# Optimization experiments

Hardware: AMD Instinct MI355X
Metric: run time of the kernel (lower is better)

Reference implementation:

```python
import jax, jax.numpy as jnp
import numpy as np

DIM = 192
HEADS = 6
HEAD_DIM = DIM // HEADS
WS = 8            # window size
N = WS * WS       # tokens per window
IN_CC = 16        # top-k kept keys per query
B, H, W = 8, 64, 64
NEG = -100.0      # value used by the torch code for masked logits
EPS_NORM = 1e-12  # F.normalize eps
EPS_LN = 1e-5     # nn.LayerNorm eps


def _rel_pos_index(ws):
    coords = np.stack(np.meshgrid(np.arange(ws), np.arange(ws), indexing='ij'))  # (2,ws,ws)
    cf = coords.reshape(2, -1)
    rel = (cf[:, :, None] - cf[:, None, :]).transpose(1, 2, 0).astype(np.int64)  # (N,N,2)
    rel[:, :, 0] += ws - 1
    rel[:, :, 1] += ws - 1
    rel[:, :, 0] *= 2 * ws - 1
    return jnp.asarray(rel.sum(-1))  # (N,N) indices into (2ws-1)^2 table

REL_IDX = _rel_pos_index(WS)


def _layer_norm(x, g, b):
    mu = jnp.mean(x, -1, keepdims=True)
    var = jnp.mean(jnp.square(x - mu), -1, keepdims=True)
    return (x - mu) * jax.lax.rsqrt(var + EPS_LN) * g + b


def _l2n(x):
    n = jnp.sqrt(jnp.sum(jnp.square(x), -1, keepdims=True))
    return x / jnp.maximum(n, EPS_NORM)


def setup_inputs() -> dict:
    key = jax.random.key(0)
    ks = jax.random.split(key, 8)
    s = 0.02
    return {
        'x': jax.random.normal(ks[0], (B, DIM, H, W), jnp.float32),
        'norm1_g': jnp.ones((DIM,), jnp.float32),
        'norm1_b': jnp.zeros((DIM,), jnp.float32),
        'qkv_w': jax.random.normal(ks[1], (3 * DIM, DIM), jnp.float32) * s,
        'qkv_b': jnp.zeros((3 * DIM,), jnp.float32),
        'proj_w': jax.random.normal(ks[2], (DIM, DIM), jnp.float32) * s,
        'proj_b': jnp.zeros((DIM,), jnp.float32),
        'rpb_table': jax.random.normal(ks[3], ((2 * WS - 1) ** 2, HEADS), jnp.float32) * s,
        'temperature': jnp.ones((HEADS, 1, 1), jnp.float32),
        'norm2_g': jnp.ones((DIM,), jnp.float32),
        'norm2_b': jnp.zeros((DIM,), jnp.float32),
        'fc1_w': jax.random.normal(ks[4], (4 * DIM, DIM), jnp.float32) * s,
        'fc1_b': jnp.zeros((4 * DIM,), jnp.float32),
        'fc2_w': jax.random.normal(ks[5], (DIM, 4 * DIM), jnp.float32) * s,
        'fc2_b': jnp.zeros((DIM,), jnp.float32),
    }


def reference(x, norm1_g, norm1_b, qkv_w, qkv_b, proj_w, proj_b, rpb_table,
              temperature, norm2_g, norm2_b, fc1_w, fc1_b, fc2_w, fc2_b):
    b, c, h, w = x.shape
    # (B,C,H,W) -> (B,L,C), pre-norm (note: the torch code norms the shortcut too)
    xs = jnp.transpose(x.reshape(b, c, h * w), (0, 2, 1))
    shortcut = _layer_norm(xs, norm1_g, norm1_b)  # (B,L,C)

    # window partition: (B,H,W,C) -> (B*nWh*nWw, N, C); shift_size=0, no padding (H,W % WS == 0)
    xin = shortcut.reshape(b, h // WS, WS, w // WS, WS, c)
    xin = jnp.transpose(xin, (0, 1, 3, 2, 4, 5)).reshape(-1, N, c)
    B_ = xin.shape[0]

    qkv = (xin @ qkv_w.T + qkv_b).reshape(B_, N, 3, HEADS, HEAD_DIM)
    qkv = jnp.transpose(qkv, (2, 0, 3, 1, 4))  # (3, B_, h, N, d)
    q, k, v = qkv[0], qkv[1], qkv[2]

    # cosine attention with learned per-head temperature
    attn = jnp.einsum('bhnd,bhmd->bhnm', _l2n(q), _l2n(k)) * temperature  # (B_,h,N,N)

    # top-k sparsification: keep IN_CC largest logits per query (threshold == kth value;
    # equivalent to the torch topk+scatter mask for distinct values)
    kth = jax.lax.top_k(attn, IN_CC)[0][..., -1:]
    attn = jnp.where(attn >= kth, attn, NEG)

    # relative position bias gather: (N,N,h) -> (h,N,N)
    rpb = jnp.transpose(rpb_table[REL_IDX], (2, 0, 1))
    attn = jax.nn.softmax(attn + rpb[None], axis=-1)

    out = jnp.einsum('bhnm,bhmd->bhnd', attn, v)
    out = jnp.transpose(out, (0, 2, 1, 3)).reshape(B_, N, c)
    out = out @ proj_w.T + proj_b

    # window reverse -> (B, L, C)
    out = out.reshape(b, h // WS, w // WS, WS, WS, c)
    out = jnp.transpose(out, (0, 1, 3, 2, 4, 5)).reshape(b, h * w, c)

    x2 = shortcut + out  # drop_path = identity (eval)
    hdn = _layer_norm(x2, norm2_g, norm2_b)
    hdn = jax.nn.gelu(hdn @ fc1_w.T + fc1_b, approximate=False) @ fc2_w.T + fc2_b
    x2 = x2 + hdn

    # back to (B,C,H,W)
    return jnp.transpose(x2, (0, 2, 1)).reshape(b, c, h, w)
```

## Files before the change

kernel.cpp:

```cpp
#include <hip/hip_runtime.h>
#include <hip/hip_bf16.h>
#include <math.h>

#define DIM     192
#define HEADS   6
#define HEAD_DIM 32
#define NTOK    64
#define IN_CC   16
#define TTOT    32768
#define NWIN    512

using bf16x8 = __attribute__((ext_vector_type(8))) short;
using f32x4  = __attribute__((ext_vector_type(4))) float;
typedef unsigned short ushort_t;

__device__ __forceinline__ ushort_t f2b(float f) {
    unsigned u = __float_as_uint(f);
    u += 0x7fffu + ((u >> 16) & 1u);
    return (ushort_t)(u >> 16);
}
__device__ __forceinline__ unsigned pk2(float a, float b) {
    return (unsigned)f2b(a) | ((unsigned)f2b(b) << 16);
}

__global__ __launch_bounds__(256) void cvt_all_kernel(
    const float* __restrict__ s0, const float* __restrict__ s1,
    const float* __restrict__ s2, const float* __restrict__ s3,
    ushort_t* __restrict__ d0, ushort_t* __restrict__ d1,
    ushort_t* __restrict__ d2, ushort_t* __restrict__ d3)
{
    const int bid = blockIdx.x;
    const float* src; ushort_t* dst; int off, K;
    if (bid < 108)      { src = s0; dst = d0; off = bid;       K = 192; }
    else if (bid < 144) { src = s1; dst = d1; off = bid - 108; K = 192; }
    else if (bid < 288) { src = s2; dst = d2; off = bid - 144; K = 192; }
    else                { src = s3; dst = d3; off = bid - 288; K = 768; }
    const int K8 = K >> 3;
    const int d  = (off * 256 + threadIdx.x) * 4;
    const int frag = d >> 7, win = d & 127;
    const int m16w = win >> 3, k7 = win & 7;
    const int oblk = frag / K8, kblk = frag - oblk * K8;
    const int o = oblk * 16 + m16w, k = kblk * 8 + k7;
    float4 v = *(const float4*)(src + (size_t)o * K + k);
    ushort4 ov;
    ov.x = f2b(v.x); ov.y = f2b(v.y); ov.z = f2b(v.z); ov.w = f2b(v.w);
    *(ushort4*)(dst + d) = ov;
}

__global__ __launch_bounds__(256) void ln1_kernel(
    const float* __restrict__ x, const float* __restrict__ g,
    const float* __restrict__ bb, float* __restrict__ outp,
    ushort_t* __restrict__ outh)
{
    __shared__ float xs[64][193];
    __shared__ float mu_s[64], rs_s[64];
    __shared__ float gs[192], bs[192];
    const int tid = threadIdx.x;
    const int t0  = blockIdx.x * 64;
    const int b   = t0 >> 12;
    const int hw0 = t0 & 4095;
    if (tid < 192) { gs[tid] = g[tid]; bs[tid] = bb[tid]; }
    const int tok = tid & 63, qq = tid >> 6;
    const float* xb = x + (size_t)b * (DIM * 4096) + hw0 + tok;
    #pragma unroll
    for (int it = 0; it < 48; ++it) {
        int c = it * 4 + qq;
        xs[tok][c] = xb[(size_t)c * 4096];
    }
    __syncthreads();
    const int tok2 = tid >> 2, p = tid & 3;
    float sum = 0.f;
    #pragma unroll
    for (int c = 0; c < 48; ++c) sum += xs[tok2][p * 48 + c];
    sum += __shfl_xor(sum, 1);
    sum += __shfl_xor(sum, 2);
    const float m = sum * (1.0f / 192.0f);
    float ss = 0.f;
    #pragma unroll
    for (int c = 0; c < 48; ++c) { float d = xs[tok2][p * 48 + c] - m; ss += d * d; }
    ss += __shfl_xor(ss, 1);
    ss += __shfl_xor(ss, 2);
    if (p == 0) {
        mu_s[tok2] = m;
        rs_s[tok2] = 1.0f / sqrtf(ss * (1.0f / 192.0f) + 1e-5f);
    }
    __syncthreads();
    float* ob = outp + (size_t)t0 * DIM;
    ushort_t* obh = outh + (size_t)t0 * DIM;
    #pragma unroll
    for (int it = 0; it < 48; ++it) {
        int idx = it * 256 + tid;
        int tk = idx / 192, c = idx % 192;
        float v = (xs[tk][c] - mu_s[tk]) * rs_s[tk] * gs[c] + bs[c];
        ob[idx] = v;
        obh[idx] = f2b(v);
    }
}

__global__ __launch_bounds__(256) void gemm_mfma(
    const ushort_t* __restrict__ A, const ushort_t* __restrict__ Wf,
    const float* __restrict__ bias, const float* __restrict__ res,
    float* __restrict__ outf, ushort_t* __restrict__ outh,
    int N, int K, int epi)
{
    __shared__ __align__(16) float Ct[4][32][68];
    const int tid  = threadIdx.x;
    const int wave = tid >> 6, lane = tid & 63;
    const int m16 = lane & 15, quad = lane >> 4;
    const int t0 = (blockIdx.x * 4 + wave) * 64, o0 = blockIdx.y * 64;
    const int K8 = K >> 3;
    float (*Cw)[68] = Ct[wave];

    f32x4 acc[4][4];
    #pragma unroll
    for (int i = 0; i < 4; ++i)
        #pragma unroll
        for (int j = 0; j < 4; ++j)
            acc[i][j] = (f32x4)(0.0f);

    const ushort_t* Ab = A + (size_t)t0 * K + quad * 8;
    const ushort_t* Wb = Wf + (size_t)(o0 >> 4) * K8 * 128 + m16 * 8;
    for (int ks = 0; ks < K; ks += 32) {
        bf16x8 af[4], wv[4];
        #pragma unroll
        for (int i = 0; i < 4; ++i)
            af[i] = *(const bf16x8*)(Ab + (size_t)(16 * i + m16) * K + ks);
        #pragma unroll
        for (int j = 0; j < 4; ++j)
            wv[j] = *(const bf16x8*)(Wb + (size_t)(j * K8 + (ks >> 3) + quad) * 128);
        #pragma unroll
        for (int i = 0; i < 4; ++i)
            #pragma unroll
            for (int j = 0; j < 4; ++j)
                acc[i][j] = __builtin_amdgcn_mfma_f32_16x16x32_bf16(wv[j], af[i], acc[i][j], 0, 0, 0);
    }

    float4 bj[4];
    #pragma unroll
    for (int j = 0; j < 4; ++j)
        bj[j] = *(const float4*)&bias[o0 + 16 * j + quad * 4];

    #pragma unroll
    for (int p = 0; p < 2; ++p) {
        #pragma unroll
        for (int ih = 0; ih < 2; ++ih) {
            const int i = 2 * p + ih;
            #pragma unroll
            for (int j = 0; j < 4; ++j) {
                f32x4 v = acc[i][j];
                v[0] += bj[j].x; v[1] += bj[j].y; v[2] += bj[j].z; v[3] += bj[j].w;
                *(f32x4*)&Cw[ih * 16 + m16][16 * j + quad * 4] = v;
            }
        }
        if (epi == 3) {
            #pragma unroll
            for (int q = 0; q < 4; ++q) {
                const int idx = q * 64 + lane;
                const int row = idx >> 3, c8 = (idx & 7) * 8;
                float4 f0 = *(const float4*)&Cw[row][c8];
                float4 f1 = *(const float4*)&Cw[row][c8 + 4];
                uint4 w;
                w.x = pk2(f0.x, f0.y); w.y = pk2(f0.z, f0.w);
                w.z = pk2(f1.x, f1.y); w.w = pk2(f1.z, f1.w);
                *(uint4*)&outh[(size_t)(t0 + p * 32 + row) * N + o0 + c8] = w;
            }
        } else {
            #pragma unroll
            for (int q = 0; q < 8; ++q) {
                const int idx = q * 64 + lane;
                const int row = idx >> 4, c4 = (idx & 15) * 4;
                float4 vv = *(const float4*)&Cw[row][c4];
                const size_t gidx = (size_t)(t0 + p * 32 + row) * N + o0 + c4;
                if (epi == 1) {
                    const float4 rv = *(const float4*)&res[gidx];
                    vv.x += rv.x; vv.y += rv.y; vv.z += rv.z; vv.w += rv.w;
                }
                *(float4*)&outf[gidx] = vv;
            }
        }
    }
}

__global__ __launch_bounds__(384) void attn_proj_fused(
    const ushort_t* __restrict__ qkvh, const float* __restrict__ rpb_table,
    const float* __restrict__ temp, const ushort_t* __restrict__ wpf,
    const float* __restrict__ proj_b, const float* __restrict__ shortcut,
    float* __restrict__ x2)
{
    __shared__ __align__(16) char smem[96768];
    const int tid  = threadIdx.x;
    const int wave = tid >> 6, n = tid & 63;
    char* arena = smem + wave * 16128;
    ushort_t* Qh  = (ushort_t*)arena;
    ushort_t* Kh  = (ushort_t*)(arena + 5120);
    float*    Ss  = (float*)arena;
    ushort_t* Pl  = (ushort_t*)arena;
    ushort_t* Vt  = (ushort_t*)(arena + 10240);
    float*    ksb = (float*)(arena + 14848);
    float*    rpb = (float*)(arena + 15104);
    ushort_t (*AoT)[200] = (ushort_t(*)[200])smem;
    float* Cww = (float*)(smem + 25600 + wave * 9216);

    const int win = blockIdx.x;
    const int h   = wave;
    const int b   = win >> 6;
    const int wh  = (win >> 3) & 7, ww = win & 7;
    const int i1  = n >> 3, j1 = n & 7;
    const int t   = b * 4096 + (wh * 8 + i1) * 64 + (ww * 8 + j1);
    const ushort_t* base = qkvh + (size_t)t * 576 + h * 32;
    const int m16 = n & 15, quad = n >> 4;

    unsigned qu[16], ku[16], vu[16];
    #pragma unroll
    for (int c = 0; c < 4; ++c) {
        ((uint4*)qu)[c] = *(const uint4*)(base + 8 * c);
        ((uint4*)ku)[c] = *(const uint4*)(base + 192 + 8 * c);
        ((uint4*)vu)[c] = *(const uint4*)(base + 384 + 8 * c);
    }
    float sq = 0.f, sk = 0.f;
    #pragma unroll
    for (int c = 0; c < 16; ++c) {
        float a0 = __uint_as_float(qu[c] << 16);
        float a1 = __uint_as_float(qu[c] & 0xffff0000u);
        sq += a0 * a0 + a1 * a1;
        float b0 = __uint_as_float(ku[c] << 16);
        float b1 = __uint_as_float(ku[c] & 0xffff0000u);
        sk += b0 * b0 + b1 * b1;
    }
    const float qs  = temp[h] / fmaxf(sqrtf(sq), 1e-12f);
    const float ksc = 1.0f / fmaxf(sqrtf(sk), 1e-12f);

    #pragma unroll
    for (int c = 0; c < 4; ++c) {
        *(uint4*)&Qh[n * 40 + 8 * c] = ((uint4*)qu)[c];
        *(uint4*)&Kh[n * 40 + 8 * c] = ((uint4*)ku)[c];
    }
    const int vslot = 4 * m16 + quad;
    #pragma unroll
    for (int d = 0; d < 16; ++d) {
        Vt[(2 * d) * 72 + vslot]     = (ushort_t)(vu[d] & 0xffffu);
        Vt[(2 * d + 1) * 72 + vslot] = (ushort_t)(vu[d] >> 16);
    }
    ksb[vslot] = ksc;
    for (int r = n; r < 225; r += 64) rpb[r] = rpb_table[r * 6 + h];
    __syncthreads();

    bf16x8 aq[4], bk[4];
    #pragma unroll
    for (int i = 0; i < 4; ++i) aq[i] = *(const bf16x8*)&Qh[(16*i + m16) * 40 + quad * 8];
    #pragma unroll
    for (int j = 0; j < 4; ++j) bk[j] = *(const bf16x8*)&Kh[(16*j + m16) * 40 + quad * 8];
    f32x4 acc[4][4];
    #pragma unroll
    for (int i = 0; i < 4; ++i)
        #pragma unroll
        for (int j = 0; j < 4; ++j)
            acc[i][j] = __builtin_amdgcn_mfma_f32_16x16x32_bf16(aq[i], bk[j], (f32x4)(0.0f), 0, 0, 0);
    __syncthreads();

    float s[64];
    #pragma unroll
    for (int i = 0; i < 2; ++i)
        #pragma unroll
        for (int r = 0; r < 4; ++r) {
            f32x4 vv = { acc[i][0][r], acc[i][1][r], acc[i][2][r], acc[i][3][r] };
            *(f32x4*)&Ss[(16 * i + 4 * quad + r) * 68 + 4 * m16] = vv;
        }
    __syncthreads();
    if (n < 32) {
        #pragma unroll
        for (int c = 0; c < 16; ++c)
            *(float4*)&s[4 * c] = *(const float4*)&Ss[n * 68 + 4 * c];
    }
    __syncthreads();
    #pragma unroll
    for (int i = 2; i < 4; ++i)
        #pragma unroll
        for (int r = 0; r < 4; ++r) {
            f32x4 vv = { acc[i][0][r], acc[i][1][r], acc[i][2][r], acc[i][3][r] };
            *(f32x4*)&Ss[(16 * (i - 2) + 4 * quad + r) * 68 + 4 * m16] = vv;
        }
    __syncthreads();
    if (n >= 32) {
        #pragma unroll
        for (int c = 0; c < 16; ++c)
            *(float4*)&s[4 * c] = *(const float4*)&Ss[(n - 32) * 68 + 4 * c];
    }

    #pragma unroll
    for (int c = 0; c < 16; ++c) {
        float4 kv = *(const float4*)&ksb[4 * c];
        s[4*c+0] *= qs * kv.x; s[4*c+1] *= qs * kv.y;
        s[4*c+2] *= qs * kv.z; s[4*c+3] *= qs * kv.w;
    }

    float thr = 1e30f;
    for (int it = 0; it < IN_CC; ++it) {
        float mx = -1e30f;
        #pragma unroll
        for (int m = 0; m < 64; ++m) {
            float vv = (s[m] < thr) ? s[m] : -1e30f;
            mx = fmaxf(mx, vv);
        }
        thr = mx;
    }

    const int basen = i1 * 15 + j1;
    float mx = -1e30f;
    #pragma unroll
    for (int c = 0; c < 64; ++c) {
        const int m = 16 * (c & 3) + (c >> 2);
        const int i2 = m >> 3, j2 = m & 7;
        float vv = ((s[c] >= thr) ? s[c] : -100.0f)
                 + rpb[basen + (7 - i2) * 15 + (7 - j2)];
        s[c] = vv;
        mx = fmaxf(mx, vv);
    }
    float sum = 0.f;
    #pragma unroll
    for (int c = 0; c < 64; ++c) { float e = __expf(s[c] - mx); s[c] = e; sum += e; }
    const float inv = 1.0f / sum;
    #pragma unroll
    for (int c = 0; c < 64; ++c) s[c] *= inv;

    __syncthreads();
    #pragma unroll
    for (int gix = 0; gix < 8; ++gix) {
        uint4 w;
        w.x = pk2(s[8*gix+0], s[8*gix+1]); w.y = pk2(s[8*gix+2], s[8*gix+3]);
        w.z = pk2(s[8*gix+4], s[8*gix+5]); w.w = pk2(s[8*gix+6], s[8*gix+7]);
        *(uint4*)&Pl[n * 72 + 8 * gix] = w;
    }
    __syncthreads();

    f32x4 o[4][2];
    #pragma unroll
    for (int i = 0; i < 4; ++i)
        #pragma unroll
        for (int j2 = 0; j2 < 2; ++j2)
            o[i][j2] = (f32x4)(0.0f);
    #pragma unroll
    for (int kh = 0; kh < 64; kh += 32) {
        bf16x8 pa[4], vb[2];
        #pragma unroll
        for (int i = 0; i < 4; ++i)
            pa[i] = *(const bf16x8*)&Pl[(16*i + m16) * 72 + kh + quad * 8];
        #pragma unroll
        for (int j2 = 0; j2 < 2; ++j2)
            vb[j2] = *(const bf16x8*)&Vt[(16*j2 + m16) * 72 + kh + quad * 8];
        #pragma unroll
        for (int i = 0; i < 4; ++i)
            #pragma unroll
            for (int j2 = 0; j2 < 2; ++j2)
                o[i][j2] = __builtin_amdgcn_mfma_f32_16x16x32_bf16(pa[i], vb[j2], o[i][j2], 0, 0, 0);
    }
    __syncthreads();

    #pragma unroll
    for (int i = 0; i < 4; ++i) {
        #pragma unroll
        for (int r = 0; r < 4; ++r) {
            const int row = 16 * i + 4 * quad + r;
            AoT[row][h * 32 + m16]      = f2b(o[i][0][r]);
            AoT[row][h * 32 + 16 + m16] = f2b(o[i][1][r]);
        }
    }
    __syncthreads();

    f32x4 pacc[4][2];
    #pragma unroll
    for (int i = 0; i < 4; ++i)
        #pragma unroll
        for (int j = 0; j < 2; ++j)
            pacc[i][j] = (f32x4)(0.0f);
    const ushort_t* Wb = wpf + (size_t)(wave * 2) * 24 * 128 + m16 * 8;
    for (int ks = 0; ks < 192; ks += 32) {
        bf16x8 af[4], wv[2];
        #pragma unroll
        for (int i = 0; i < 4; ++i)
            af[i] = *(const bf16x8*)&AoT[16 * i + m16][quad * 8 + ks];
        #pragma unroll
        for (int j = 0; j < 2; ++j)
            wv[j] = *(const bf16x8*)(Wb + (size_t)(j * 24 + (ks >> 3) + quad) * 128);
        #pragma unroll
        for (int i = 0; i < 4; ++i)
            #pragma unroll
            for (int j = 0; j < 2; ++j)
                pacc[i][j] = __builtin_amdgcn_mfma_f32_16x16x32_bf16(wv[j], af[i], pacc[i][j], 0, 0, 0);
    }

    float4 bj[2];
    #pragma unroll
    for (int j = 0; j < 2; ++j)
        bj[j] = *(const float4*)&proj_b[wave * 32 + 16 * j + quad * 4];
    #pragma unroll
    for (int i = 0; i < 4; ++i)
        #pragma unroll
        for (int j = 0; j < 2; ++j) {
            f32x4 v = pacc[i][j];
            v[0] += bj[j].x; v[1] += bj[j].y; v[2] += bj[j].z; v[3] += bj[j].w;
            *(f32x4*)&Cww[(16 * i + m16) * 36 + 16 * j + quad * 4] = v;
        }

    #pragma unroll
    for (int q = 0; q < 8; ++q) {
        const int idx = q * 64 + n;
        const int row = idx >> 3, c4 = (idx & 7) * 4;
        const int ii = row >> 3, jj = row & 7;
        const int tt = b * 4096 + (wh * 8 + ii) * 64 + ww * 8 + jj;
        float4 vv = *(const float4*)&Cww[row * 36 + c4];
        const float4 rv = *(const float4*)&shortcut[(size_t)tt * DIM + wave * 32 + c4];
        vv.x += rv.x; vv.y += rv.y; vv.z += rv.z; vv.w += rv.w;
        *(float4*)&x2[(size_t)tt * DIM + wave * 32 + c4] = vv;
    }
}

__global__ __launch_bounds__(256) void mlp_fused(
    const float* __restrict__ x2, const ushort_t* __restrict__ w1f,
    const ushort_t* __restrict__ w2f, const float* __restrict__ fc1_b,
    const float* __restrict__ fc2_b, const float* __restrict__ g2,
    const float* __restrict__ b2, float* __restrict__ outp)
{
    __shared__ __align__(16) char smem[43008];
    ushort_t (*h_h)[200] = (ushort_t(*)[200])smem;
    ushort_t (*a1c)[136] = (ushort_t(*)[136])(smem + 25600);
    float* gs  = (float*)(smem + 25600);
    float* bs  = gs + 192;

    const int tid  = threadIdx.x;
    const int wave = tid >> 6, lane = tid & 63;
    const int m16 = lane & 15, quad = lane >> 4;
    const int t0 = blockIdx.x * 64;
    const int b   = t0 >> 12;
    const int hw0 = t0 & 4095;

    if (tid < 192) { gs[tid] = g2[tid]; bs[tid] = b2[tid]; }
    __syncthreads();
    {
        const int tok = tid >> 2, p = tid & 3;
        const float* rp = x2 + (size_t)(t0 + tok) * DIM + p * 48;
        float xv[48];
        #pragma unroll
        for (int c4 = 0; c4 < 12; ++c4)
            *(float4*)&xv[c4 * 4] = *(const float4*)(rp + c4 * 4);
        float sum = 0.f;
        #pragma unroll
        for (int c = 0; c < 48; ++c) sum += xv[c];
        sum += __shfl_xor(sum, 1);
        sum += __shfl_xor(sum, 2);
        const float m = sum * (1.0f / 192.0f);
        float ss = 0.f;
        #pragma unroll
        for (int c = 0; c < 48; ++c) { float d = xv[c] - m; ss += d * d; }
        ss += __shfl_xor(ss, 1);
        ss += __shfl_xor(ss, 2);
        const float rs = 1.0f / sqrtf(ss * (1.0f / 192.0f) + 1e-5f);
        ushort_t* hp = &h_h[tok][p * 48];
        #pragma unroll
        for (int c2 = 0; c2 < 24; ++c2) {
            float v0 = (xv[2*c2]   - m) * rs * gs[p * 48 + 2*c2]   + bs[p * 48 + 2*c2];
            float v1 = (xv[2*c2+1] - m) * rs * gs[p * 48 + 2*c2+1] + bs[p * 48 + 2*c2+1];
            *(unsigned*)(hp + 2 * c2) = pk2(v0, v1);
        }
    }
    __syncthreads();

    f32x4 acc2[4][3];
    #pragma unroll
    for (int i = 0; i < 4; ++i)
        #pragma unroll
        for (int j = 0; j < 3; ++j)
            acc2[i][j] = (f32x4)(0.0f);

    for (int c = 0; c < 6; ++c) {
        f32x4 acc1[4][2];
        #pragma unroll
        for (int i = 0; i < 4; ++i)
            #pragma unroll
            for (int j = 0; j < 2; ++j)
                acc1[i][j] = (f32x4)(0.0f);
        const ushort_t* Wb1 = w1f + (size_t)(c * 8 + wave * 2) * 24 * 128 + m16 * 8;
        for (int ks = 0; ks < 192; ks += 32) {
            bf16x8 af[4], wv[2];
            #pragma unroll
            for (int i = 0; i < 4; ++i)
                af[i] = *(const bf16x8*)&h_h[16 * i + m16][quad * 8 + ks];
            #pragma unroll
            for (int j = 0; j < 2; ++j)
                wv[j] = *(const bf16x8*)(Wb1 + (size_t)(j * 24 + (ks >> 3) + quad) * 128);
            #pragma unroll
            for (int i = 0; i < 4; ++i)
                #pragma unroll
                for (int j = 0; j < 2; ++j)
                    acc1[i][j] = __builtin_amdgcn_mfma_f32_16x16x32_bf16(wv[j], af[i], acc1[i][j], 0, 0, 0);
        }
        #pragma unroll
        for (int j = 0; j < 2; ++j) {
            const int o = c * 128 + wave * 32 + 16 * j + quad * 4;
            const float4 bv = *(const float4*)&fc1_b[o];
            #pragma unroll
            for (int i = 0; i < 4; ++i) {
                f32x4 v = acc1[i][j];
                v[0] += bv.x; v[1] += bv.y; v[2] += bv.z; v[3] += bv.w;
                #pragma unroll
                for (int r = 0; r < 4; ++r) {
                    float xg = v[r];
                    float e1 = __expf(xg * (1.5957691f + 0.0713548f * xg * xg)) + 1.0f;
                    v[r] = xg - xg * __builtin_amdgcn_rcpf(e1);
                }
                uint2 pkd;
                pkd.x = pk2(v[0], v[1]); pkd.y = pk2(v[2], v[3]);
                *(uint2*)&a1c[16 * i + m16][wave * 32 + 16 * j + quad * 4] = pkd;
            }
        }
        __syncthreads();
        const ushort_t* Wb2 = w2f + (size_t)(wave * 3) * 96 * 128 + m16 * 8;
        for (int ks = 0; ks < 128; ks += 32) {
            bf16x8 af2[4], wv2[3];
            #pragma unroll
            for (int i = 0; i < 4; ++i)
                af2[i] = *(const bf16x8*)&a1c[16 * i + m16][quad * 8 + ks];
            #pragma unroll
            for (int j = 0; j < 3; ++j)
                wv2[j] = *(const bf16x8*)(Wb2 + (size_t)(j * 96 + c * 16 + (ks >> 3) + quad) * 128);
            #pragma unroll
            for (int i = 0; i < 4; ++i)
                #pragma unroll
                for (int j = 0; j < 3; ++j)
                    acc2[i][j] = __builtin_amdgcn_mfma_f32_16x16x32_bf16(wv2[j], af2[i], acc2[i][j], 0, 0, 0);
        }
        __syncthreads();
    }

    float (*Cw)[68] = (float(*)[68])(smem + wave * 8704);
    float4 b2j[3];
    #pragma unroll
    for (int j = 0; j < 3; ++j)
        b2j[j] = *(const float4*)&fc2_b[wave * 48 + 16 * j + quad * 4];
    #pragma unroll
    for (int p = 0; p < 2; ++p) {
        #pragma unroll
        for (int ih = 0; ih < 2; ++ih) {
            const int i = 2 * p + ih;
            #pragma unroll
            for (int j = 0; j < 3; ++j) {
                f32x4 v = acc2[i][j];
                v[0] += b2j[j].x; v[1] += b2j[j].y; v[2] += b2j[j].z; v[3] += b2j[j].w;
                *(f32x4*)&Cw[ih * 16 + m16][16 * j + quad * 4] = v;
            }
        }
        #pragma unroll
        for (int q = 0; q < 6; ++q) {
            const int idx = q * 64 + lane;
            const int cc = idx >> 3, t4 = (idx & 7) * 4;
            const int o  = wave * 48 + cc;
            const int tb = t0 + p * 32 + t4;
            float4 vv;
            vv.x = Cw[t4 + 0][cc] + x2[(size_t)(tb + 0) * DIM + o];
            vv.y = Cw[t4 + 1][cc] + x2[(size_t)(tb + 1) * DIM + o];
            vv.z = Cw[t4 + 2][cc] + x2[(size_t)(tb + 2) * DIM + o];
            vv.w = Cw[t4 + 3][cc] + x2[(size_t)(tb + 3) * DIM + o];
            *(float4*)&outp[(size_t)b * (DIM * 4096) + (size_t)o * 4096
                            + hw0 + p * 32 + t4] = vv;
        }
    }
}

extern "C" void kernel_launch(void* const* d_in, const int* in_sizes, int n_in,
                              void* d_out, int out_size, void* d_ws, size_t ws_size,
                              hipStream_t stream)
{
    const float* x        = (const float*)d_in[0];
    const float* norm1_g  = (const float*)d_in[1];
    const float* norm1_b  = (const float*)d_in[2];
    const float* qkv_w    = (const float*)d_in[3];
    const float* qkv_b    = (const float*)d_in[4];
    const float* proj_w   = (const float*)d_in[5];
    const float* proj_b   = (const float*)d_in[6];
    const float* rpbt     = (const float*)d_in[7];
    const float* temp     = (const float*)d_in[8];
    const float* norm2_g  = (const float*)d_in[9];
    const float* norm2_b  = (const float*)d_in[10];
    const float* fc1_w    = (const float*)d_in[11];
    const float* fc1_b    = (const float*)d_in[12];
    const float* fc2_w    = (const float*)d_in[13];
    const float* fc2_b    = (const float*)d_in[14];
    float* out = (float*)d_out;

    char* wsb = (char*)d_ws;
    float*    shortcut   = (float*)wsb;
    ushort_t* shortcut_h = (ushort_t*)(wsb + 25165824);
    ushort_t* qkvh       = (ushort_t*)(wsb + 37748736);
    float*    x2         = (float*)(wsb + 88080384);
    ushort_t* wq  = (ushort_t*)(wsb + 125829120);
    ushort_t* wp  = wq + 110592;
    ushort_t* w1  = wp + 36864;
    ushort_t* w2  = w1 + 147456;

    hipLaunchKernelGGL(cvt_all_kernel, dim3(432), dim3(256), 0, stream,
                       qkv_w, proj_w, fc1_w, fc2_w, wq, wp, w1, w2);

    hipLaunchKernelGGL(ln1_kernel, dim3(TTOT / 64), dim3(256), 0, stream,
                       x, norm1_g, norm1_b, shortcut, shortcut_h);
    hipLaunchKernelGGL(gemm_mfma, dim3(TTOT / 256, 9), dim3(256), 0, stream,
                       shortcut_h, wq, qkv_b, (const float*)nullptr,
                       (float*)nullptr, qkvh, 576, 192, 3);
    hipLaunchKernelGGL(attn_proj_fused, dim3(NWIN), dim3(384), 0, stream,
                       qkvh, rpbt, temp, wp, proj_b, shortcut, x2);
    hipLaunchKernelGGL(mlp_fused, dim3(TTOT / 64), dim3(256), 0, stream,
                       x2, w1, w2, fc1_b, fc2_b, norm2_g, norm2_b, out);
}
```

Before: 217.3 us.

## Fuse QKV projection into windowed attention kernel and drop fp32 shortcut

Moves the QKV GEMM inside the per-window attention kernel, where each wave computes its head's Q, K and V directly into shared memory. This removes the separate GEMM launch and the large bf16 qkv intermediate. The LayerNorm kernel no longer writes an fp32 shortcut; the residual is read from the bf16 normalized tensor, trading precision for bandwidth. Several block barriers are removed, relying on per-wave private shared arenas.

```diff
diff --git a/kernel.cpp b/kernel.cpp
--- a/kernel.cpp
+++ b/kernel.cpp
@@ -21,6 +21,9 @@
 }
 __device__ __forceinline__ unsigned pk2(float a, float b) {
     return (unsigned)f2b(a) | ((unsigned)f2b(b) << 16);
+}
+__device__ __forceinline__ float b2f(ushort_t u) {
+    return __uint_as_float(((unsigned)u) << 16);
 }
 
 __global__ __launch_bounds__(256) void cvt_all_kernel(
@@ -49,8 +52,7 @@
 
 __global__ __launch_bounds__(256) void ln1_kernel(
     const float* __restrict__ x, const float* __restrict__ g,
-    const float* __restrict__ bb, float* __restrict__ outp,
-    ushort_t* __restrict__ outh)
+    const float* __restrict__ bb, ushort_t* __restrict__ outh)
 {
     __shared__ float xs[64][193];
     __shared__ float mu_s[64], rs_s[64];
@@ -85,119 +87,33 @@
         rs_s[tok2] = 1.0f / sqrtf(ss * (1.0f / 192.0f) + 1e-5f);
     }
     __syncthreads();
-    float* ob = outp + (size_t)t0 * DIM;
     ushort_t* obh = outh + (size_t)t0 * DIM;
     #pragma unroll
     for (int it = 0; it < 48; ++it) {
         int idx = it * 256 + tid;
         int tk = idx / 192, c = idx % 192;
-        float v = (xs[tk][c] - mu_s[tk]) * rs_s[tk] * gs[c] + bs[c];
-        ob[idx] = v;
-        obh[idx] = f2b(v);
-    }
-}
-
-__global__ __launch_bounds__(256) void gemm_mfma(
-    const ushort_t* __restrict__ A, const ushort_t* __restrict__ Wf,
-    const float* __restrict__ bias, const float* __restrict__ res,
-    float* __restrict__ outf, ushort_t* __restrict__ outh,
-    int N, int K, int epi)
+        obh[idx] = f2b((xs[tk][c] - mu_s[tk]) * rs_s[tk] * gs[c] + bs[c]);
+    }
+}
+
+__global__ __launch_bounds__(384) void attn_fused(
+    const ushort_t* __restrict__ sc_h, const ushort_t* __restrict__ wqf,
+    const float* __restrict__ qkv_b, const float* __restrict__ rpb_table,
+    const float* __restrict__ temp, const ushort_t* __restrict__ wpf,
+    const float* __restrict__ proj_b, float* __restrict__ x2)
 {
-    __shared__ __align__(16) float Ct[4][32][68];
-    const int tid  = threadIdx.x;
-    const int wave = tid >> 6, lane = tid & 63;
-    const int m16 = lane & 15, quad = lane >> 4;
-    const int t0 = (blockIdx.x * 4 + wave) * 64, o0 = blockIdx.y * 64;
-    const int K8 = K >> 3;
-    float (*Cw)[68] = Ct[wave];
-
-    f32x4 acc[4][4];
-    #pragma unroll
-    for (int i = 0; i < 4; ++i)
-        #pragma unroll
-        for (int j = 0; j < 4; ++j)
-            acc[i][j] = (f32x4)(0.0f);
-
-    const ushort_t* Ab = A + (size_t)t0 * K + quad * 8;
-    const ushort_t* Wb = Wf + (size_t)(o0 >> 4) * K8 * 128 + m16 * 8;
-    for (int ks = 0; ks < K; ks += 32) {
-        bf16x8 af[4], wv[4];
-        #pragma unroll
-        for (int i = 0; i < 4; ++i)
-            af[i] = *(const bf16x8*)(Ab + (size_t)(16 * i + m16) * K + ks);
-        #pragma unroll
-        for (int j = 0; j < 4; ++j)
-            wv[j] = *(const bf16x8*)(Wb + (size_t)(j * K8 + (ks >> 3) + quad) * 128);
-        #pragma unroll
-        for (int i = 0; i < 4; ++i)
-            #pragma unroll
-            for (int j = 0; j < 4; ++j)
-                acc[i][j] = __builtin_amdgcn_mfma_f32_16x16x32_bf16(wv[j], af[i], acc[i][j], 0, 0, 0);
-    }
-
-    float4 bj[4];
-    #pragma unroll
-    for (int j = 0; j < 4; ++j)
-        bj[j] = *(const float4*)&bias[o0 + 16 * j + quad * 4];
-
-    #pragma unroll
-    for (int p = 0; p < 2; ++p) {
-        #pragma unroll
-        for (int ih = 0; ih < 2; ++ih) {
-            const int i = 2 * p + ih;
-            #pragma unroll
-            for (int j = 0; j < 4; ++j) {
-                f32x4 v = acc[i][j];
-                v[0] += bj[j].x; v[1] += bj[j].y; v[2] += bj[j].z; v[3] += bj[j].w;
-                *(f32x4*)&Cw[ih * 16 + m16][16 * j + quad * 4] = v;
-            }
-        }
-        if (epi == 3) {
-            #pragma unroll
-            for (int q = 0; q < 4; ++q) {
-                const int idx = q * 64 + lane;
-                const int row = idx >> 3, c8 = (idx & 7) * 8;
-                float4 f0 = *(const float4*)&Cw[row][c8];
-                float4 f1 = *(const float4*)&Cw[row][c8 + 4];
-                uint4 w;
-                w.x = pk2(f0.x, f0.y); w.y = pk2(f0.z, f0.w);
-                w.z = pk2(f1.x, f1.y); w.w = pk2(f1.z, f1.w);
-                *(uint4*)&outh[(size_t)(t0 + p * 32 + row) * N + o0 + c8] = w;
-            }
-        } else {
-            #pragma unroll
-            for (int q = 0; q < 8; ++q) {
-                const int idx = q * 64 + lane;
-                const int row = idx >> 4, c4 = (idx & 15) * 4;
-                float4 vv = *(const float4*)&Cw[row][c4];
-                const size_t gidx = (size_t)(t0 + p * 32 + row) * N + o0 + c4;
-                if (epi == 1) {
-                    const float4 rv = *(const float4*)&res[gidx];
-                    vv.x += rv.x; vv.y += rv.y; vv.z += rv.z; vv.w += rv.w;
-                }
-                *(float4*)&outf[gidx] = vv;
-            }
-        }
-    }
-}
-
-__global__ __launch_bounds__(384) void attn_proj_fused(
-    const ushort_t* __restrict__ qkvh, const float* __restrict__ rpb_table,
-    const float* __restrict__ temp, const ushort_t* __restrict__ wpf,
-    const float* __restrict__ proj_b, const float* __restrict__ shortcut,
-    float* __restrict__ x2)
-{
-    __shared__ __align__(16) char smem[96768];
+    __shared__ __align__(16) char smem[98304];
     const int tid  = threadIdx.x;
     const int wave = tid >> 6, n = tid & 63;
-    char* arena = smem + wave * 16128;
+    char* arena = smem + wave * 16384;
     ushort_t* Qh  = (ushort_t*)arena;
     ushort_t* Kh  = (ushort_t*)(arena + 5120);
     float*    Ss  = (float*)arena;
     ushort_t* Pl  = (ushort_t*)arena;
     ushort_t* Vt  = (ushort_t*)(arena + 10240);
     float*    ksb = (float*)(arena + 14848);
-    float*    rpb = (float*)(arena + 15104);
+    float*    qnb = (float*)(arena + 15104);
+    float*    rpb = (float*)(arena + 15360);
     ushort_t (*AoT)[200] = (ushort_t(*)[200])smem;
     float* Cww = (float*)(smem + 25600 + wave * 9216);
 
@@ -206,44 +122,82 @@
     const int b   = win >> 6;
     const int wh  = (win >> 3) & 7, ww = win & 7;
     const int i1  = n >> 3, j1 = n & 7;
-    const int t   = b * 4096 + (wh * 8 + i1) * 64 + (ww * 8 + j1);
-    const ushort_t* base = qkvh + (size_t)t * 576 + h * 32;
     const int m16 = n & 15, quad = n >> 4;
 
-    unsigned qu[16], ku[16], vu[16];
-    #pragma unroll
-    for (int c = 0; c < 4; ++c) {
-        ((uint4*)qu)[c] = *(const uint4*)(base + 8 * c);
-        ((uint4*)ku)[c] = *(const uint4*)(base + 192 + 8 * c);
-        ((uint4*)vu)[c] = *(const uint4*)(base + 384 + 8 * c);
-    }
-    float sq = 0.f, sk = 0.f;
-    #pragma unroll
-    for (int c = 0; c < 16; ++c) {
-        float a0 = __uint_as_float(qu[c] << 16);
-        float a1 = __uint_as_float(qu[c] & 0xffff0000u);
-        sq += a0 * a0 + a1 * a1;
-        float b0 = __uint_as_float(ku[c] << 16);
-        float b1 = __uint_as_float(ku[c] & 0xffff0000u);
-        sk += b0 * b0 + b1 * b1;
-    }
-    const float qs  = temp[h] / fmaxf(sqrtf(sq), 1e-12f);
-    const float ksc = 1.0f / fmaxf(sqrtf(sk), 1e-12f);
-
-    #pragma unroll
-    for (int c = 0; c < 4; ++c) {
-        *(uint4*)&Qh[n * 40 + 8 * c] = ((uint4*)qu)[c];
-        *(uint4*)&Kh[n * 40 + 8 * c] = ((uint4*)ku)[c];
-    }
-    const int vslot = 4 * m16 + quad;
-    #pragma unroll
-    for (int d = 0; d < 16; ++d) {
-        Vt[(2 * d) * 72 + vslot]     = (ushort_t)(vu[d] & 0xffffu);
-        Vt[(2 * d + 1) * 72 + vslot] = (ushort_t)(vu[d] >> 16);
-    }
-    ksb[vslot] = ksc;
     for (int r = n; r < 225; r += 64) rpb[r] = rpb_table[r * 6 + h];
-    __syncthreads();
+
+    int trow[4];
+    #pragma unroll
+    for (int i = 0; i < 4; ++i) {
+        const int row = 16 * i + m16;
+        trow[i] = b * 4096 + (wh * 8 + (row >> 3)) * 64 + ww * 8 + (row & 7);
+    }
+
+    #pragma unroll
+    for (int part = 0; part < 3; ++part) {
+        const int o0 = part * 192 + h * 32;
+        f32x4 pa[4][2];
+        #pragma unroll
+        for (int i = 0; i < 4; ++i)
+            #pragma unroll
+            for (int j = 0; j < 2; ++j)
+                pa[i][j] = (f32x4)(0.0f);
+        const ushort_t* Wb = wqf + (size_t)(o0 >> 4) * 24 * 128 + m16 * 8;
+        for (int ks = 0; ks < 192; ks += 32) {
+            bf16x8 af[4], wv[2];
+            #pragma unroll
+            for (int i = 0; i < 4; ++i)
+                af[i] = *(const bf16x8*)(sc_h + (size_t)trow[i] * 192 + ks + quad * 8);
+            #pragma unroll
+            for (int j = 0; j < 2; ++j)
+                wv[j] = *(const bf16x8*)(Wb + (size_t)(j * 24 + (ks >> 3) + quad) * 128);
+            #pragma unroll
+            for (int i = 0; i < 4; ++i)
+                #pragma unroll
+                for (int j = 0; j < 2; ++j)
+                    pa[i][j] = __builtin_amdgcn_mfma_f32_16x16x32_bf16(wv[j], af[i], pa[i][j], 0, 0, 0);
+        }
+        float4 bv0 = *(const float4*)&qkv_b[o0 + quad * 4];
+        float4 bv1 = *(const float4*)&qkv_b[o0 + 16 + quad * 4];
+        float ssq[4] = {0.f, 0.f, 0.f, 0.f};
+        #pragma unroll
+        for (int i = 0; i < 4; ++i) {
+            f32x4 v0 = pa[i][0], v1 = pa[i][1];
+            v0[0] += bv0.x; v0[1] += bv0.y; v0[2] += bv0.z; v0[3] += bv0.w;
+            v1[0] += bv1.x; v1[1] += bv1.y; v1[2] += bv1.z; v1[3] += bv1.w;
+            if (part < 2) {
+                #pragma unroll
+                for (int r = 0; r < 4; ++r)
+                    ssq[i] += v0[r] * v0[r] + v1[r] * v1[r];
+                ushort_t* dst = (part == 0) ? Qh : Kh;
+                uint2 w0, w1;
+                w0.x = pk2(v0[0], v0[1]); w0.y = pk2(v0[2], v0[3]);
+                w1.x = pk2(v1[0], v1[1]); w1.y = pk2(v1[2], v1[3]);
+                *(uint2*)&dst[(16 * i + m16) * 40 + quad * 4]      = w0;
+                *(uint2*)&dst[(16 * i + m16) * 40 + 16 + quad * 4] = w1;
+            } else {
+                #pragma unroll
+                for (int r = 0; r < 4; ++r) {
+                    Vt[(quad * 4 + r) * 72 + 4 * m16 + i]      = f2b(v0[r]);
+                    Vt[(16 + quad * 4 + r) * 72 + 4 * m16 + i] = f2b(v1[r]);
+                }
+            }
+        }
+        if (part < 2) {
+            #pragma unroll
+            for (int i = 0; i < 4; ++i) {
+                ssq[i] += __shfl_xor(ssq[i], 16);
+                ssq[i] += __shfl_xor(ssq[i], 32);
+            }
+            if (quad == 0) {
+                #pragma unroll
+                for (int i = 0; i < 4; ++i) {
+                    if (part == 0) qnb[16 * i + m16] = ssq[i];
+                    else           ksb[4 * m16 + i]  = 1.0f / fmaxf(sqrtf(ssq[i]), 1e-12f);
+                }
+            }
+        }
+    }
 
     bf16x8 aq[4], bk[4];
     #pragma unroll
@@ -256,7 +210,6 @@
         #pragma unroll
         for (int j = 0; j < 4; ++j)
             acc[i][j] = __builtin_amdgcn_mfma_f32_16x16x32_bf16(aq[i], bk[j], (f32x4)(0.0f), 0, 0, 0);
-    __syncthreads();
 
     float s[64];
     #pragma unroll
@@ -266,13 +219,11 @@
             f32x4 vv = { acc[i][0][r], acc[i][1][r], acc[i][2][r], acc[i][3][r] };
             *(f32x4*)&Ss[(16 * i + 4 * quad + r) * 68 + 4 * m16] = vv;
         }
-    __syncthreads();
     if (n < 32) {
         #pragma unroll
         for (int c = 0; c < 16; ++c)
             *(float4*)&s[4 * c] = *(const float4*)&Ss[n * 68 + 4 * c];
     }
-    __syncthreads();
     #pragma unroll
     for (int i = 2; i < 4; ++i)
         #pragma unroll
@@ -280,13 +231,13 @@
             f32x4 vv = { acc[i][0][r], acc[i][1][r], acc[i][2][r], acc[i][3][r] };
             *(f32x4*)&Ss[(16 * (i - 2) + 4 * quad + r) * 68 + 4 * m16] = vv;
         }
-    __syncthreads();
     if (n >= 32) {
         #pragma unroll
         for (int c = 0; c < 16; ++c)
             *(float4*)&s[4 * c] = *(const float4*)&Ss[(n - 32) * 68 + 4 * c];
     }
 
+    const float qs = temp[h] / fmaxf(sqrtf(qnb[n]), 1e-12f);
     #pragma unroll
     for (int c = 0; c < 16; ++c) {
         float4 kv = *(const float4*)&ksb[4 * c];
@@ -323,7 +274,6 @@
     #pragma unroll
     for (int c = 0; c < 64; ++c) s[c] *= inv;
 
-    __syncthreads();
     #pragma unroll
     for (int gix = 0; gix < 8; ++gix) {
         uint4 w;
@@ -331,7 +281,6 @@
         w.z = pk2(s[8*gix+4], s[8*gix+5]); w.w = pk2(s[8*gix+6], s[8*gix+7]);
         *(uint4*)&Pl[n * 72 + 8 * gix] = w;
     }
-    __syncthreads();
 
     f32x4 o[4][2];
     #pragma unroll
@@ -409,8 +358,11 @@
         const int ii = row >> 3, jj = row & 7;
         const int tt = b * 4096 + (wh * 8 + ii) * 64 + ww * 8 + jj;
         float4 vv = *(const float4*)&Cww[row * 36 + c4];
-        const float4 rv = *(const float4*)&shortcut[(size_t)tt * DIM + wave * 32 + c4];
-        vv.x += rv.x; vv.y += rv.y; vv.z += rv.z; vv.w += rv.w;
+        uint2 rv = *(const uint2*)&sc_h[(size_t)tt * 192 + wave * 32 + c4];
+        vv.x += b2f((ushort_t)(rv.x & 0xffffu));
+        vv.y += b2f((ushort_t)(rv.x >> 16));
+        vv.z += b2f((ushort_t)(rv.y & 0xffffu));
+        vv.w += b2f((ushort_t)(rv.y >> 16));
         *(float4*)&x2[(size_t)tt * DIM + wave * 32 + c4] = vv;
     }
 }
@@ -588,10 +540,8 @@
     float* out = (float*)d_out;
 
     char* wsb = (char*)d_ws;
-    float*    shortcut   = (float*)wsb;
-    ushort_t* shortcut_h = (ushort_t*)(wsb + 25165824);
-    ushort_t* qkvh       = (ushort_t*)(wsb + 37748736);
-    float*    x2         = (float*)(wsb + 88080384);
+    ushort_t* shortcut_h = (ushort_t*)wsb;
+    float*    x2         = (float*)(wsb + 12582912);
     ushort_t* wq  = (ushort_t*)(wsb + 125829120);
     ushort_t* wp  = wq + 110592;
     ushort_t* w1  = wp + 36864;
@@ -601,12 +551,9 @@
                        qkv_w, proj_w, fc1_w, fc2_w, wq, wp, w1, w2);
 
     hipLaunchKernelGGL(ln1_kernel, dim3(TTOT / 64), dim3(256), 0, stream,
-                       x, norm1_g, norm1_b, shortcut, shortcut_h);
-    hipLaunchKernelGGL(gemm_mfma, dim3(TTOT / 256, 9), dim3(256), 0, stream,
-                       shortcut_h, wq, qkv_b, (const float*)nullptr,
-                       (float*)nullptr, qkvh, 576, 192, 3);
-    hipLaunchKernelGGL(attn_proj_fused, dim3(NWIN), dim3(384), 0, stream,
-                       qkvh, rpbt, temp, wp, proj_b, shortcut, x2);
+                       x, norm1_g, norm1_b, shortcut_h);
+    hipLaunchKernelGGL(attn_fused, dim3(NWIN), dim3(384), 0, stream,
+                       shortcut_h, wq, qkv_b, rpbt, temp, wp, proj_b, x2);
     hipLaunchKernelGGL(mlp_fused, dim3(TTOT / 64), dim3(256), 0, stream,
                        x2, w1, w2, fc1_b, fc2_b, norm2_g, norm2_b, out);
 }
```

Result: faster. 212.0 us (-2.4%).
